# Performance work log

Hardware: AMD Instinct MI355X
Metric: run time of the kernel (lower is better)

Reference implementation:

```python
import jax, jax.numpy as jnp
import numpy as np

N_HEADS, D_MODEL, D_HEAD = 16, 1024, 64
BATCH, SEQ = 8, 1024
INIT_RANGE = 0.02
IGNORE = -100000.0


def setup_inputs() -> dict:
    key = jax.random.key(0)
    ks = jax.random.split(key, 6)
    return {
        "normalized_resid_pre": jax.random.normal(ks[0], (BATCH, SEQ, D_MODEL), jnp.float32),
        "encoder_output": jax.random.normal(ks[1], (BATCH, SEQ, D_MODEL), jnp.float32),
        "Qs": jax.random.normal(ks[2], (N_HEADS, D_MODEL, D_HEAD), jnp.float32) * INIT_RANGE,
        "Qbs": jnp.zeros((N_HEADS, D_HEAD), jnp.float32),
        "Ks": jax.random.normal(ks[3], (N_HEADS, D_MODEL, D_HEAD), jnp.float32) * INIT_RANGE,
        "Kbs": jnp.zeros((N_HEADS, D_HEAD), jnp.float32),
        "Vs": jax.random.normal(ks[4], (N_HEADS, D_MODEL, D_HEAD), jnp.float32) * INIT_RANGE,
        "Vbs": jnp.zeros((N_HEADS, D_HEAD), jnp.float32),
        "O": jax.random.normal(ks[5], (N_HEADS, D_HEAD, D_MODEL), jnp.float32) * INIT_RANGE,
        "Ob": jnp.zeros((D_MODEL,), jnp.float32),
    }


def reference(normalized_resid_pre, encoder_output, Qs, Qbs, Ks, Kbs, Vs, Vbs, O, Ob):
    sqrt_d_head = np.sqrt(D_HEAD).astype(np.float32)
    # per-head projections: q,k from encoder_output, v from normalized_resid_pre
    q = jnp.einsum('bpd,hdk->bphk', encoder_output, Qs) + Qbs
    k = jnp.einsum('bpd,hdk->bphk', encoder_output, Ks) + Kbs
    v = jnp.einsum('bpd,hdk->bphk', normalized_resid_pre, Vs) + Vbs
    # [B,H,Q,K] scores, scaled then causally masked with -1e5 (not -inf)
    scores = jnp.einsum('bqhk,bmhk->bhqm', q, k) / sqrt_d_head
    causal = jnp.triu(jnp.ones((SEQ, SEQ), bool), k=1)
    scores = jnp.where(causal, jnp.float32(IGNORE), scores)
    attn = jax.nn.softmax(scores, axis=-1)
    z = jnp.einsum('bmhk,bhqm->bqhk', v, attn)
    return jnp.einsum('bqhk,hkd->bqd', z, O) + Ob
```

## Files before the change

### kernel.cpp

```cpp
#include <hip/hip_runtime.h>
#include <hip/hip_bf16.h>
#include <cstdint>
#include <cstddef>


typedef __attribute__((ext_vector_type(8))) short short8;
typedef __attribute__((ext_vector_type(4))) short short4v;
typedef __attribute__((ext_vector_type(4))) float f32x4;

#define MFMA16(A, B, C) __builtin_amdgcn_mfma_f32_16x16x32_bf16(A, B, C, 0, 0, 0)

__device__ inline short f2bs(float f) {
    __bf16 h = (__bf16)f;
    return __builtin_bit_cast(short, h);
}

typedef const __attribute__((address_space(1))) unsigned int* as1_u32p;
typedef __attribute__((address_space(3))) unsigned int* as3_u32p;

__device__ inline void gload_lds16(const void* g, void* lds_base) {
    __builtin_amdgcn_global_load_lds((as1_u32p)(uintptr_t)g,
                                     (as3_u32p)(uintptr_t)lds_base, 16, 0, 0);
}

__global__ __launch_bounds__(256) void cvt_k(const float* __restrict__ a,
                                             const float* __restrict__ b,
                                             short* __restrict__ oa,
                                             short* __restrict__ ob) {
    const int n = 8 * 1024 * 1024;
    const float* src = blockIdx.y ? b : a;
    short* dst = blockIdx.y ? ob : oa;
    for (int i = (blockIdx.x * 256 + threadIdx.x) * 8; i < n; i += gridDim.x * 256 * 8) {
        f32x4 v0 = *(const f32x4*)(src + i), v1 = *(const f32x4*)(src + i + 4);
        short8 o;
        o[0] = f2bs(v0[0]); o[1] = f2bs(v0[1]); o[2] = f2bs(v0[2]); o[3] = f2bs(v0[3]);
        o[4] = f2bs(v1[0]); o[5] = f2bs(v1[1]); o[6] = f2bs(v1[2]); o[7] = f2bs(v1[3]);
        *(short8*)(dst + i) = o;
    }
}

__global__ __launch_bounds__(256) void wtrans_k(
    const float* __restrict__ Wq, const float* __restrict__ Wk,
    const float* __restrict__ Wv, const float* __restrict__ Wo,
    short* __restrict__ TQ, short* __restrict__ TK,
    short* __restrict__ TV, short* __restrict__ TO) {
    __shared__ short tile[64][72];
    const int wsel = blockIdx.y;
    const float* in = wsel == 0 ? Wq : wsel == 1 ? Wk : wsel == 2 ? Wv : Wo;
    short* out = wsel == 0 ? TQ : wsel == 1 ? TK : wsel == 2 ? TV : TO;
    const int h = blockIdx.x >> 4, tk = blockIdx.x & 15;
    const int t = threadIdx.x;
    size_t ioff; int istr, orow0, ocol0;
    if (wsel < 3) { ioff = (size_t)h * 65536 + (size_t)tk * 64 * 64; istr = 64;   orow0 = h * 64;  ocol0 = tk * 64; }
    else          { ioff = (size_t)h * 65536 + (size_t)tk * 64;      istr = 1024; orow0 = tk * 64; ocol0 = h * 64; }
    {
        const int r = t >> 2, c0 = (t & 3) * 16;
        const float* src = in + ioff + (size_t)r * istr + c0;
#pragma unroll
        for (int j = 0; j < 4; j++) {
            f32x4 v = *(const f32x4*)(src + j * 4);
            tile[r][c0 + j * 4 + 0] = f2bs(v[0]);
            tile[r][c0 + j * 4 + 1] = f2bs(v[1]);
            tile[r][c0 + j * 4 + 2] = f2bs(v[2]);
            tile[r][c0 + j * 4 + 3] = f2bs(v[3]);
        }
    }
    __syncthreads();
    {
        const int cc = t >> 2, rb = (t & 3) * 16;
        short8 o0, o1;
#pragma unroll
        for (int j = 0; j < 8; j++) { o0[j] = tile[rb + j][cc]; o1[j] = tile[rb + 8 + j][cc]; }
        short* dst = out + (size_t)(orow0 + cc) * 1024 + ocol0 + rb;
        *(short8*)dst = o0;
        *(short8*)(dst + 8) = o1;
    }
}

template <int MODE>
__global__ __launch_bounds__(256) void gemm_bt(const short* __restrict__ A,
                                               const short* __restrict__ B,
                                               const float* __restrict__ bias,
                                               void* __restrict__ Cp) {
    constexpr int K = 1024;
    __shared__ short As[128 * 64];
    __shared__ short Bs[128 * 64];
    const int t = threadIdx.x, l = t & 63, w = t >> 6, lr = l & 15, lg = l >> 4;
    const int wm = (w >> 1) * 64, wn = (w & 1) * 64;
    const int m0 = blockIdx.x * 128, n0 = blockIdx.y * 128;
    const int sr = l >> 3, cb = l & 7;
    f32x4 acc[4][4] = {};

    for (int k0 = 0; k0 < K; k0 += 64) {
#pragma unroll
        for (int i = 0; i < 4; i++) {
            const int c = w * 4 + i, r = c * 8 + sr, cbs = cb ^ (r & 7);
            gload_lds16(A + (size_t)(m0 + r) * K + k0 + cbs * 8, &As[c * 512]);
        }
#pragma unroll
        for (int i = 0; i < 4; i++) {
            const int c = w * 4 + i, r = c * 8 + sr, cbs = cb ^ (r & 7);
            gload_lds16(B + (size_t)(n0 + r) * K + k0 + cbs * 8, &Bs[c * 512]);
        }
        __syncthreads();
#pragma unroll
        for (int kk = 0; kk < 2; kk++) {
            short8 af[4], bf[4];
#pragma unroll
            for (int mi = 0; mi < 4; mi++) {
                const int r = wm + mi * 16 + lr;
                af[mi] = *(const short8*)&As[r * 64 + ((kk * 4 + lg) ^ (r & 7)) * 8];
            }
#pragma unroll
            for (int nj = 0; nj < 4; nj++) {
                const int r = wn + nj * 16 + lr;
                bf[nj] = *(const short8*)&Bs[r * 64 + ((kk * 4 + lg) ^ (r & 7)) * 8];
            }
#pragma unroll
            for (int mi = 0; mi < 4; mi++)
#pragma unroll
                for (int nj = 0; nj < 4; nj++)
                    acc[mi][nj] = MFMA16(af[mi], bf[nj], acc[mi][nj]);
        }
        __syncthreads();
    }

#pragma unroll
    for (int mi = 0; mi < 4; mi++) {
#pragma unroll
        for (int nj = 0; nj < 4; nj++) {
            const int col = n0 + wn + nj * 16 + lr;
            const float bv = bias[col];
            if (MODE == 2) {
                const int rowb = m0 + wm + mi * 16 + lg * 4;
                const int bb = rowb >> 10, s0 = rowb & 1023;
                const int h = col >> 6, d = col & 63;
                short4v pk;
#pragma unroll
                for (int e = 0; e < 4; e++) pk[e] = f2bs(acc[mi][nj][e] + bv);
                *(short4v*)((short*)Cp + ((size_t)(bb * 16 + h) * 64 + d) * 1024 + s0) = pk;
            } else {
#pragma unroll
                for (int e = 0; e < 4; e++) {
                    const int row = m0 + wm + mi * 16 + lg * 4 + e;
                    const float val = acc[mi][nj][e] + bv;
                    if (MODE == 1) {
                        const int bb = row >> 10, s = row & 1023;
                        const int h = col >> 6, d = col & 63;
                        ((short*)Cp)[((size_t)(bb * 16 + h) * 1024 + s) * 64 + d] = f2bs(val);
                    } else {
                        ((float*)Cp)[(size_t)row * 1024 + col] = val;
                    }
                }
            }
        }
    }
}

__global__ __launch_bounds__(256) void attn_k(const short* __restrict__ Q,
                                              const short* __restrict__ Kp,
                                              const short* __restrict__ Vg,
                                              short* __restrict__ Z) {
    __shared__ short Ks[64 * 64];
    __shared__ short Vt[64 * 64];
    __shared__ short Ps[4][16][72];
    const int t = threadIdx.x, l = t & 63, w = t >> 6, lr = l & 15, lg = l >> 4;
    const int bh = blockIdx.x, qb = 15 - blockIdx.y, q0 = qb * 64;
    const size_t base = (size_t)bh * 65536;
    const int sr = l >> 3, cb = l & 7;

    short8 qf[2];
    {
        const short* qp = Q + base + (size_t)(q0 + w * 16 + lr) * 64 + lg * 8;
        qf[0] = *(const short8*)qp;
        qf[1] = *(const short8*)(qp + 32);
    }

    float mrun[4], lsum[4];
    f32x4 acc[4] = {};
#pragma unroll
    for (int e = 0; e < 4; e++) { mrun[e] = -1e30f; lsum[e] = 0.f; }

    for (int kt = 0; kt <= qb; kt++) {
        const int k0 = kt * 64;
#pragma unroll
        for (int i = 0; i < 2; i++) {
            const int c = w * 2 + i, r = c * 8 + sr, cbs = cb ^ (r & 7);
            gload_lds16(Kp + base + (size_t)(k0 + r) * 64 + cbs * 8, &Ks[c * 512]);
            gload_lds16(Vg + base + (size_t)r * 1024 + k0 + cbs * 8, &Vt[c * 512]);
        }
        __syncthreads();

        f32x4 sf[4];
#pragma unroll
        for (int n = 0; n < 4; n++) {
            const int rk = n * 16 + lr;
            short8 kf0 = *(const short8*)&Ks[rk * 64 + ((lg) ^ (rk & 7)) * 8];
            short8 kf1 = *(const short8*)&Ks[rk * 64 + ((4 + lg) ^ (rk & 7)) * 8];
            f32x4 s = {};
            s = MFMA16(qf[0], kf0, s);
            s = MFMA16(qf[1], kf1, s);
            sf[n] = s;
        }

        const bool diag = (kt == qb);
        float pr[4][4];
#pragma unroll
        for (int e = 0; e < 4; e++) {
            float vals[4];
#pragma unroll
            for (int n = 0; n < 4; n++) {
                float x = sf[n][e] * 0.125f;
                if (diag && (n * 16 + lr > w * 16 + lg * 4 + e)) x = -1e30f;
                vals[n] = x;
            }
            float tm = fmaxf(fmaxf(vals[0], vals[1]), fmaxf(vals[2], vals[3]));
#pragma unroll
            for (int off = 1; off < 16; off <<= 1)
                tm = fmaxf(tm, __shfl_xor(tm, off));
            float nm = fmaxf(mrun[e], tm);
            float alpha = __expf(mrun[e] - nm);
            mrun[e] = nm;
            float rs = 0.f;
#pragma unroll
            for (int n = 0; n < 4; n++) {
                float p = __expf(vals[n] - nm);
                pr[e][n] = p;
                rs += p;
            }
#pragma unroll
            for (int off = 1; off < 16; off <<= 1)
                rs += __shfl_xor(rs, off);
            lsum[e] = lsum[e] * alpha + rs;
#pragma unroll
            for (int n4 = 0; n4 < 4; n4++) acc[n4][e] *= alpha;
        }
#pragma unroll
        for (int e = 0; e < 4; e++)
#pragma unroll
            for (int n = 0; n < 4; n++)
                Ps[w][lg * 4 + e][n * 16 + lr] = f2bs(pr[e][n]);

#pragma unroll
        for (int c = 0; c < 2; c++) {
            short8 pf = *(const short8*)&Ps[w][lr][lg * 8 + c * 32];
#pragma unroll
            for (int n4 = 0; n4 < 4; n4++) {
                const int rv = n4 * 16 + lr;
                short8 vf = *(const short8*)&Vt[rv * 64 + ((lg + 4 * c) ^ (rv & 7)) * 8];
                acc[n4] = MFMA16(pf, vf, acc[n4]);
            }
        }
        __syncthreads();
    }

    const int b = bh >> 4, h = bh & 15;
    float rec[4];
#pragma unroll
    for (int e = 0; e < 4; e++) rec[e] = 1.f / lsum[e];
#pragma unroll
    for (int n4 = 0; n4 < 4; n4++)
#pragma unroll
        for (int e = 0; e < 4; e++) {
            const int row = q0 + w * 16 + lg * 4 + e;
            Z[((size_t)(b * 1024 + row)) * 1024 + h * 64 + n4 * 16 + lr] =
                f2bs(acc[n4][e] * rec[e]);
        }
}

extern "C" void kernel_launch(void* const* d_in, const int* in_sizes, int n_in,
                              void* d_out, int out_size, void* d_ws, size_t ws_size,
                              hipStream_t stream) {
    const float* resid = (const float*)d_in[0];
    const float* enc   = (const float*)d_in[1];
    const float* Qs    = (const float*)d_in[2];
    const float* Qbs   = (const float*)d_in[3];
    const float* Ksw   = (const float*)d_in[4];
    const float* Kbs   = (const float*)d_in[5];
    const float* Vs    = (const float*)d_in[6];
    const float* Vbs   = (const float*)d_in[7];
    const float* Ow    = (const float*)d_in[8];
    const float* Ob    = (const float*)d_in[9];
    float* out = (float*)d_out;

    char* ws = (char*)d_ws;
    const size_t M16 = (size_t)16 * 1024 * 1024;
    short* Aenc = (short*)ws;
    short* Ares = (short*)(ws + M16);
    short* Qw   = (short*)(ws + 2 * M16);
    short* Kw   = (short*)(ws + 3 * M16);
    short* Vw   = (short*)(ws + 4 * M16);
    short* WqT  = (short*)(ws + 5 * M16);
    short* WkT  = (short*)(ws + 5 * M16 + 2 * 1024 * 1024);
    short* WvT  = (short*)(ws + 5 * M16 + 4 * 1024 * 1024);
    short* WoT  = (short*)(ws + 5 * M16 + 6 * 1024 * 1024);
    short* Zw   = Aenc;

    cvt_k<<<dim3(2048, 2), 256, 0, stream>>>(enc, resid, Aenc, Ares);
    wtrans_k<<<dim3(256, 4), 256, 0, stream>>>(Qs, Ksw, Vs, Ow, WqT, WkT, WvT, WoT);
    gemm_bt<1><<<dim3(64, 8), 256, 0, stream>>>(Aenc, WqT, Qbs, Qw);
    gemm_bt<1><<<dim3(64, 8), 256, 0, stream>>>(Aenc, WkT, Kbs, Kw);
    gemm_bt<2><<<dim3(64, 8), 256, 0, stream>>>(Ares, WvT, Vbs, Vw);
    attn_k<<<dim3(128, 16), 256, 0, stream>>>(Qw, Kw, Vw, Zw);
    gemm_bt<0><<<dim3(64, 8), 256, 0, stream>>>(Zw, WoT, Ob, out);
}
```

Measured before the change: 177.9 us.

## Pair causal query blocks per workgroup and add lazy softmax rescaling

Each workgroup now processes two query blocks (qb and 15-qb), so every block does the same number of K/V tiles and each loaded K/V tile is reused by both query tiles. The launch grid is halved to match. Softmax moves to exp2 with the scale folded in, and the running max is only updated when a new max exceeds the old one by a threshold (checked wave-wide). The per-row sum reduction across lanes is deferred to the end, and launch bounds now request 4 blocks per CU. This cuts causal load imbalance, redundant K/V loads and per-tile shuffle work, at the cost of more registers per thread and possible precision loss from the delayed rescaling.

```diff
diff --git a/kernel.cpp b/kernel.cpp
--- a/kernel.cpp
+++ b/kernel.cpp
@@ -2,6 +2,7 @@
 #include <hip/hip_bf16.h>
 #include <cstdint>
 #include <cstddef>
+#include <math.h>
 
 
 typedef __attribute__((ext_vector_type(8))) short short8;
@@ -157,31 +158,108 @@
     }
 }
 
-__global__ __launch_bounds__(256) void attn_k(const short* __restrict__ Q,
-                                              const short* __restrict__ Kp,
-                                              const short* __restrict__ Vg,
-                                              short* __restrict__ Z) {
+#define ATTN_THR 11.5415603f
+
+__device__ __forceinline__ void attn_tile(
+    const short* __restrict__ Ks, const short* __restrict__ Vt,
+    short (*__restrict__ Psw)[72],
+    const short8* __restrict__ qf, float* __restrict__ m,
+    float* __restrict__ ps, f32x4* __restrict__ acc,
+    bool diag, int lr, int lg, int rowloc) {
+    f32x4 sf[4];
+#pragma unroll
+    for (int n = 0; n < 4; n++) {
+        const int rk = n * 16 + lr;
+        short8 kf0 = *(const short8*)&Ks[rk * 64 + ((lg) ^ (rk & 7)) * 8];
+        short8 kf1 = *(const short8*)&Ks[rk * 64 + ((4 + lg) ^ (rk & 7)) * 8];
+        f32x4 s = {};
+        s = MFMA16(qf[0], kf0, s);
+        s = MFMA16(qf[1], kf1, s);
+        sf[n] = s;
+    }
+    const float SC = 0.18033688f;
+#pragma unroll
+    for (int n = 0; n < 4; n++)
+#pragma unroll
+        for (int e = 0; e < 4; e++) {
+            float x = sf[n][e] * SC;
+            if (diag && (n * 16 + lr > rowloc + e)) x = -1e30f;
+            sf[n][e] = x;
+        }
+    float pm[4];
+#pragma unroll
+    for (int e = 0; e < 4; e++)
+        pm[e] = fmaxf(fmaxf(sf[0][e], sf[1][e]), fmaxf(sf[2][e], sf[3][e]));
+    bool ok = true;
+#pragma unroll
+    for (int e = 0; e < 4; e++) ok = ok && (pm[e] <= m[e] + ATTN_THR);
+    if (!__all(ok)) {
+#pragma unroll
+        for (int e = 0; e < 4; e++) {
+            float tm = pm[e];
+#pragma unroll
+            for (int off = 1; off < 16; off <<= 1)
+                tm = fmaxf(tm, __shfl_xor(tm, off));
+            float nm = fmaxf(m[e], tm);
+            float al = exp2f(m[e] - nm);
+            m[e] = nm;
+            ps[e] *= al;
+#pragma unroll
+            for (int n4 = 0; n4 < 4; n4++) acc[n4][e] *= al;
+        }
+    }
+#pragma unroll
+    for (int e = 0; e < 4; e++) {
+#pragma unroll
+        for (int n = 0; n < 4; n++) {
+            float p = exp2f(sf[n][e] - m[e]);
+            ps[e] += p;
+            Psw[lg * 4 + e][n * 16 + lr] = f2bs(p);
+        }
+    }
+#pragma unroll
+    for (int c = 0; c < 2; c++) {
+        short8 pf = *(const short8*)&Psw[lr][lg * 8 + c * 32];
+#pragma unroll
+        for (int n4 = 0; n4 < 4; n4++) {
+            const int rv = n4 * 16 + lr;
+            short8 vf = *(const short8*)&Vt[rv * 64 + ((lg + 4 * c) ^ (rv & 7)) * 8];
+            acc[n4] = MFMA16(pf, vf, acc[n4]);
+        }
+    }
+}
+
+__global__ __launch_bounds__(256, 4) void attn_k(const short* __restrict__ Q,
+                                                 const short* __restrict__ Kp,
+                                                 const short* __restrict__ Vg,
+                                                 short* __restrict__ Z) {
     __shared__ short Ks[64 * 64];
     __shared__ short Vt[64 * 64];
     __shared__ short Ps[4][16][72];
     const int t = threadIdx.x, l = t & 63, w = t >> 6, lr = l & 15, lg = l >> 4;
-    const int bh = blockIdx.x, qb = 15 - blockIdx.y, q0 = qb * 64;
+    const int bh = blockIdx.x;
+    const int qbA = blockIdx.y, qbB = 15 - qbA;
+    const int q0A = qbA * 64, q0B = qbB * 64;
     const size_t base = (size_t)bh * 65536;
     const int sr = l >> 3, cb = l & 7;
-
-    short8 qf[2];
+    const int rowloc = w * 16 + lg * 4;
+
+    short8 qfA[2], qfB[2];
     {
-        const short* qp = Q + base + (size_t)(q0 + w * 16 + lr) * 64 + lg * 8;
-        qf[0] = *(const short8*)qp;
-        qf[1] = *(const short8*)(qp + 32);
-    }
-
-    float mrun[4], lsum[4];
-    f32x4 acc[4] = {};
-#pragma unroll
-    for (int e = 0; e < 4; e++) { mrun[e] = -1e30f; lsum[e] = 0.f; }
-
-    for (int kt = 0; kt <= qb; kt++) {
+        const short* qp = Q + base + (size_t)(q0A + w * 16 + lr) * 64 + lg * 8;
+        qfA[0] = *(const short8*)qp;
+        qfA[1] = *(const short8*)(qp + 32);
+        qp = Q + base + (size_t)(q0B + w * 16 + lr) * 64 + lg * 8;
+        qfB[0] = *(const short8*)qp;
+        qfB[1] = *(const short8*)(qp + 32);
+    }
+
+    float mA[4], mB[4], psA[4], psB[4];
+    f32x4 accA[4] = {}, accB[4] = {};
+#pragma unroll
+    for (int e = 0; e < 4; e++) { mA[e] = mB[e] = -1e30f; psA[e] = psB[e] = 0.f; }
+
+    for (int kt = 0; kt <= qbB; kt++) {
         const int k0 = kt * 64;
 #pragma unroll
         for (int i = 0; i < 2; i++) {
@@ -190,81 +268,33 @@
             gload_lds16(Vg + base + (size_t)r * 1024 + k0 + cbs * 8, &Vt[c * 512]);
         }
         __syncthreads();
-
-        f32x4 sf[4];
-#pragma unroll
-        for (int n = 0; n < 4; n++) {
-            const int rk = n * 16 + lr;
-            short8 kf0 = *(const short8*)&Ks[rk * 64 + ((lg) ^ (rk & 7)) * 8];
-            short8 kf1 = *(const short8*)&Ks[rk * 64 + ((4 + lg) ^ (rk & 7)) * 8];
-            f32x4 s = {};
-            s = MFMA16(qf[0], kf0, s);
-            s = MFMA16(qf[1], kf1, s);
-            sf[n] = s;
-        }
-
-        const bool diag = (kt == qb);
-        float pr[4][4];
+        if (kt <= qbA)
+            attn_tile(Ks, Vt, Ps[w], qfA, mA, psA, accA, kt == qbA, lr, lg, rowloc);
+        attn_tile(Ks, Vt, Ps[w], qfB, mB, psB, accB, kt == qbB, lr, lg, rowloc);
+        __syncthreads();
+    }
+
+    const int b = bh >> 4, h = bh & 15;
+#pragma unroll
+    for (int e = 0; e < 4; e++) {
+        float sA = psA[e], sB = psB[e];
+#pragma unroll
+        for (int off = 1; off < 16; off <<= 1) {
+            sA += __shfl_xor(sA, off);
+            sB += __shfl_xor(sB, off);
+        }
+        psA[e] = 1.f / sA;
+        psB[e] = 1.f / sB;
+    }
+#pragma unroll
+    for (int n4 = 0; n4 < 4; n4++)
 #pragma unroll
         for (int e = 0; e < 4; e++) {
-            float vals[4];
-#pragma unroll
-            for (int n = 0; n < 4; n++) {
-                float x = sf[n][e] * 0.125f;
-                if (diag && (n * 16 + lr > w * 16 + lg * 4 + e)) x = -1e30f;
-                vals[n] = x;
-            }
-            float tm = fmaxf(fmaxf(vals[0], vals[1]), fmaxf(vals[2], vals[3]));
-#pragma unroll
-            for (int off = 1; off < 16; off <<= 1)
-                tm = fmaxf(tm, __shfl_xor(tm, off));
-            float nm = fmaxf(mrun[e], tm);
-            float alpha = __expf(mrun[e] - nm);
-            mrun[e] = nm;
-            float rs = 0.f;
-#pragma unroll
-            for (int n = 0; n < 4; n++) {
-                float p = __expf(vals[n] - nm);
-                pr[e][n] = p;
-                rs += p;
-            }
-#pragma unroll
-            for (int off = 1; off < 16; off <<= 1)
-                rs += __shfl_xor(rs, off);
-            lsum[e] = lsum[e] * alpha + rs;
-#pragma unroll
-            for (int n4 = 0; n4 < 4; n4++) acc[n4][e] *= alpha;
-        }
-#pragma unroll
-        for (int e = 0; e < 4; e++)
-#pragma unroll
-            for (int n = 0; n < 4; n++)
-                Ps[w][lg * 4 + e][n * 16 + lr] = f2bs(pr[e][n]);
-
-#pragma unroll
-        for (int c = 0; c < 2; c++) {
-            short8 pf = *(const short8*)&Ps[w][lr][lg * 8 + c * 32];
-#pragma unroll
-            for (int n4 = 0; n4 < 4; n4++) {
-                const int rv = n4 * 16 + lr;
-                short8 vf = *(const short8*)&Vt[rv * 64 + ((lg + 4 * c) ^ (rv & 7)) * 8];
-                acc[n4] = MFMA16(pf, vf, acc[n4]);
-            }
-        }
-        __syncthreads();
-    }
-
-    const int b = bh >> 4, h = bh & 15;
-    float rec[4];
-#pragma unroll
-    for (int e = 0; e < 4; e++) rec[e] = 1.f / lsum[e];
-#pragma unroll
-    for (int n4 = 0; n4 < 4; n4++)
-#pragma unroll
-        for (int e = 0; e < 4; e++) {
-            const int row = q0 + w * 16 + lg * 4 + e;
-            Z[((size_t)(b * 1024 + row)) * 1024 + h * 64 + n4 * 16 + lr] =
-                f2bs(acc[n4][e] * rec[e]);
+            const int rloc = w * 16 + lg * 4 + e;
+            Z[((size_t)(b * 1024 + q0A + rloc)) * 1024 + h * 64 + n4 * 16 + lr] =
+                f2bs(accA[n4][e] * psA[e]);
+            Z[((size_t)(b * 1024 + q0B + rloc)) * 1024 + h * 64 + n4 * 16 + lr] =
+                f2bs(accB[n4][e] * psB[e]);
         }
 }
 
@@ -301,6 +331,6 @@
     gemm_bt<1><<<dim3(64, 8), 256, 0, stream>>>(Aenc, WqT, Qbs, Qw);
     gemm_bt<1><<<dim3(64, 8), 256, 0, stream>>>(Aenc, WkT, Kbs, Kw);
     gemm_bt<2><<<dim3(64, 8), 256, 0, stream>>>(Ares, WvT, Vbs, Vw);
-    attn_k<<<dim3(128, 16), 256, 0, stream>>>(Qw, Kw, Vw, Zw);
+    attn_k<<<dim3(128, 8), 256, 0, stream>>>(Qw, Kw, Vw, Zw);
     gemm_bt<0><<<dim3(64, 8), 256, 0, stream>>>(Zw, WoT, Ob, out);
 }
```

Measured after the change: 163.5 us. -8.1%, faster.
